# Optimization experiments

Hardware: AMD Instinct MI355X
Metric: run time of the kernel (lower is better)

## Reference

```python
import jax, jax.numpy as jnp
import numpy as np

D_DYN = 256    # dynamic_dim
D_STAT = 64    # static_dim
U_DIM = 48     # config.model.u_dim
N_OBS = 80     # num_prod*2 + num_inj = 32*2 + 16
T = 128        # rollout steps
B = 2048       # batch


def setup_inputs() -> dict:
    key = jax.random.key(0)
    k = jax.random.split(key, 8)
    z_dyn = jax.random.normal(k[0], (B, D_DYN), dtype=jnp.float32)
    z_static = jax.random.normal(k[1], (B, D_STAT), dtype=jnp.float32)
    dt = jnp.ones((1,), dtype=jnp.float32) * 0.05
    U = jax.random.normal(k[2], (T, B, U_DIM), dtype=jnp.float32)
    # learned params, initialized as in the torch module
    eig_raw = jnp.zeros((D_DYN,), dtype=jnp.float32)
    V = jnp.eye(D_DYN, dtype=jnp.float32) + jax.random.normal(k[3], (D_DYN, D_DYN), dtype=jnp.float32) * 0.01
    L = jax.random.normal(k[4], (D_DYN, U_DIM), dtype=jnp.float32) * (1.0 / np.sqrt(U_DIM))
    C = jax.random.normal(k[5], (N_OBS, D_DYN), dtype=jnp.float32) * (1.0 / np.sqrt(D_DYN))
    Dm = jax.random.normal(k[6], (N_OBS, U_DIM), dtype=jnp.float32) * (1.0 / np.sqrt(U_DIM))
    return {"z_dyn": z_dyn, "z_static": z_static, "dt": dt, "U": U,
            "eig_raw": eig_raw, "V": V, "L": L, "C": C, "Dm": Dm}


def reference(z_dyn, z_static, dt, U, eig_raw, V, L, C, Dm):
    # Stable Koopman operator: K = V diag(sigmoid(eig_raw)*0.99) V^{-1}
    eigvals = jax.nn.sigmoid(eig_raw) * 0.99
    K = (V * eigvals[None, :]) @ jnp.linalg.inv(V)  # [d, d]
    KT, LT, CT, DT = K.T, L.T, C.T, Dm.T
    dts = dt[0]

    def step(z, ut):
        ut_dt = ut * dts                 # [B, u_dim]
        z = z @ KT + ut_dt @ LT          # [B, d]
        y = z @ CT + ut_dt @ DT          # [B, n_obs]
        return z, (z, y)

    _, (Z, Y) = jax.lax.scan(step, z_dyn, U)
    return Z, Y  # [T, B, d], [T, B, n_obs]
```

## Files before the change

kernel.cpp:

```cpp
#include <hip/hip_runtime.h>

#define D_   256
#define UD_  48
#define NO_  80
#define T_   128
#define B_   2048

typedef __bf16 bf16x8 __attribute__((ext_vector_type(8)));
typedef float  f32x4  __attribute__((ext_vector_type(4)));
typedef unsigned short ushort_t;

static __device__ __forceinline__ ushort_t f2bf(float f){
  return __builtin_bit_cast(ushort_t, (__bf16)f);
}
static __device__ __forceinline__ float bf2f(ushort_t u){
  union { unsigned int i; float f; } c; c.i = ((unsigned int)u) << 16; return c.f;
}
static __device__ __forceinline__ f32x4 mfma16(bf16x8 a, bf16x8 b, f32x4 c){
  return __builtin_amdgcn_mfma_f32_16x16x32_bf16(a, b, c, 0, 0, 0);
}


__global__ void k_init(const float* __restrict__ V, const float* __restrict__ eig,
                       float* __restrict__ Xa, float* __restrict__ lam){
  const int i = blockIdx.x, j = threadIdx.x;
  Xa[i*D_ + j] = (i == j ? 2.0f : 0.0f) - V[i*D_ + j];
  if (j == 0) lam[i] = 0.99f / (1.0f + expf(-eig[i]));
}

__global__ void k_mm_mul(const float* __restrict__ A, const float* __restrict__ B,
                         float* __restrict__ Cm){
  const int i = blockIdx.x, j = threadIdx.x;
  const float* Ar = A + i*D_;
  float a0=0.f,a1=0.f,a2=0.f,a3=0.f;
  #pragma unroll 4
  for (int k = 0; k < D_; k += 4){
    a0 += Ar[k+0] * B[(k+0)*D_ + j];
    a1 += Ar[k+1] * B[(k+1)*D_ + j];
    a2 += Ar[k+2] * B[(k+2)*D_ + j];
    a3 += Ar[k+3] * B[(k+3)*D_ + j];
  }
  Cm[i*D_ + j] = (a0+a1)+(a2+a3);
}

__global__ void k_mm_upd(const float* __restrict__ X, const float* __restrict__ Tm,
                         float* __restrict__ Xn){
  const int i = blockIdx.x, j = threadIdx.x;
  const float* Xr = X + i*D_;
  float a0=0.f,a1=0.f,a2=0.f,a3=0.f;
  #pragma unroll 4
  for (int k = 0; k < D_; k += 4){
    a0 += Xr[k+0] * Tm[(k+0)*D_ + j];
    a1 += Xr[k+1] * Tm[(k+1)*D_ + j];
    a2 += Xr[k+2] * Tm[(k+2)*D_ + j];
    a3 += Xr[k+3] * Tm[(k+3)*D_ + j];
  }
  Xn[i*D_ + j] = 2.0f*Xr[j] - ((a0+a1)+(a2+a3));
}

__global__ void k_prep1(const float* __restrict__ Vinv, const float* __restrict__ V,
                        const float* __restrict__ Lm, const float* __restrict__ Cmat,
                        const float* __restrict__ dt,
                        float* __restrict__ VinvT, float* __restrict__ Lw,
                        float* __restrict__ Cw, float* __restrict__ dVd){
  const int bid = blockIdx.x, tid = threadIdx.x;
  if (bid < 256){
    VinvT[tid*D_ + bid] = Vinv[bid*D_ + tid];
    if (tid == bid){ float v = V[bid*D_ + bid]; dVd[bid] = v - bf2f(f2bf(v)); }
  } else if (bid < 512){
    const int i = bid - 256;
    if (tid < UD_){
      float acc = 0.f;
      #pragma unroll 4
      for (int j = 0; j < D_; ++j) acc += Vinv[i*D_ + j] * Lm[j*UD_ + tid];
      Lw[i*UD_ + tid] = acc * dt[0];
    }
  } else {
    const int n = bid - 512;
    float acc = 0.f;
    #pragma unroll 4
    for (int j = 0; j < D_; ++j) acc += Cmat[n*D_ + j] * V[j*D_ + tid];
    Cw[n*D_ + tid] = acc;
  }
}

__global__ void k_prep2(const float* __restrict__ z0, const float* __restrict__ VinvT,
                        const float* __restrict__ Lw,
                        ushort_t* __restrict__ Wchk, ushort_t* __restrict__ Lws){
  __shared__ float zr[8][256];
  const int bid = blockIdx.x, tid = threadIdx.x;
  if (bid < 256){
    const int b0 = bid * 8;
    #pragma unroll
    for (int r = 0; r < 8; ++r) zr[r][tid] = z0[(size_t)(b0+r)*D_ + tid];
    __syncthreads();
    float acc[8] = {0.f,0.f,0.f,0.f,0.f,0.f,0.f,0.f};
    #pragma unroll 4
    for (int j = 0; j < D_; ++j){
      const float vj = VinvT[j*D_ + tid];
      #pragma unroll
      for (int r = 0; r < 8; ++r) acc[r] += zr[r][j] * vj;
    }
    #pragma unroll
    for (int r = 0; r < 8; ++r)
      Wchk[(size_t)(b0+r)*D_ + tid] = f2bf(acc[r]);
    return;
  }
  const int f = bid - 256;
  if (tid >= 64) return;
  const int l = tid, lm = l & 15, lh = l >> 4;
  const int it = f >> 1, kc2 = f & 1;
  const int ig = it*16 + lm;
  #pragma unroll
  for (int j = 0; j < 8; ++j){
    const int k = 32*kc2 + 4*lh + (j & 3) + 16*(j >> 2);
    Lws[(f*64 + l)*8 + j] = f2bf(k < UD_ ? Lw[ig*UD_ + k] : 0.f);
  }
}

__global__ void k_packA(const float* __restrict__ V, const float* __restrict__ Cw,
                        const float* __restrict__ Dmat, const float* __restrict__ dt,
                        ushort_t* __restrict__ Af){
  const int mt = blockIdx.x / 10, kc = blockIdx.x % 10;
  const int l = threadIdx.x, lm = l & 15, lh = l >> 4;
  const float dts = dt[0];
  #pragma unroll
  for (int j = 0; j < 8; ++j){
    const int k = 32*kc + 4*lh + (j & 3) + 16*(j >> 2);
    float val = 0.f;
    if (mt < 16){
      if (kc < 8) val = V[(mt*16 + lm)*D_ + k];
    } else {
      const int n = (mt - 16)*16 + lm;
      if (kc < 8) val = Cw[n*D_ + k];
      else { const int ku = k - 256; if (ku < UD_) val = dts * Dmat[n*UD_ + ku]; }
    }
    Af[((size_t)(mt*10 + kc)*64 + l)*8 + j] = f2bf(val);
  }
}

#define SCAN_STEP(UA, UB, UC, TT) do {                                          \
  union { ushort_t us[8]; bf16x8 v; } c0, c1;                                   \
  c0.us[0]=f2bf((UA).x); c0.us[1]=f2bf((UA).y); c0.us[2]=f2bf((UA).z); c0.us[3]=f2bf((UA).w); \
  c0.us[4]=f2bf((UB).x); c0.us[5]=f2bf((UB).y); c0.us[6]=f2bf((UB).z); c0.us[7]=f2bf((UB).w); \
  c1.us[0]=f2bf((UC).x); c1.us[1]=f2bf((UC).y); c1.us[2]=f2bf((UC).z); c1.us[3]=f2bf((UC).w); \
  c1.us[4]=0; c1.us[5]=0; c1.us[6]=0; c1.us[7]=0;                               \
  _Pragma("unroll")                                                             \
  for (int q = 0; q < 2; ++q){                                                  \
    f32x4 acc = {0.f,0.f,0.f,0.f};                                              \
    acc = mfma16(lwf[q*2+0], c0.v, acc);                                        \
    acc = mfma16(lwf[q*2+1], c1.v, acc);                                        \
    _Pragma("unroll")                                                           \
    for (int r = 0; r < 4; ++r) w[q*4+r] = lamr[q*4+r]*w[q*4+r] + acc[r];       \
  }                                                                             \
  if ((((TT) & 7) == 7) && ((TT) < T_-1)){                                      \
    const int c2 = ((TT)+1) >> 3;                                               \
    _Pragma("unroll")                                                           \
    for (int q = 0; q < 2; ++q){                                                \
      const int i = (itb+q)*16 + 4*lh;                                          \
      ushort4 o; o.x=f2bf(w[q*4+0]); o.y=f2bf(w[q*4+1]); o.z=f2bf(w[q*4+2]); o.w=f2bf(w[q*4+3]); \
      *(ushort4*)(Wchk + ((size_t)c2*B_ + row)*D_ + i) = o;                     \
    }                                                                           \
  }                                                                             \
} while(0)

__global__ void __launch_bounds__(256) k_scan(const float* __restrict__ U,
    const ushort_t* __restrict__ Lws, const float* __restrict__ lam,
    ushort_t* __restrict__ Wchk){
  const int tid = threadIdx.x;
  const int wid = tid >> 6, l = tid & 63;
  const int lm = l & 15, lh = l >> 4;
  const int bq = blockIdx.x >> 1, ih = blockIdx.x & 1;
  const int b0 = bq * 16;
  const int row = b0 + lm;
  const int itb = ih*8 + wid*2;

  bf16x8 lwf[4];
  #pragma unroll
  for (int q = 0; q < 2; ++q)
    #pragma unroll
    for (int c = 0; c < 2; ++c)
      lwf[q*2 + c] = *(const bf16x8*)(Lws + ((size_t)(((itb+q)*2 + c)*64 + l))*8);

  float lamr[8], w[8];
  #pragma unroll
  for (int q = 0; q < 2; ++q){
    const int i = (itb+q)*16 + 4*lh;
    const float4 lv = *(const float4*)&lam[i];
    const ushort4 wu = *(const ushort4*)(Wchk + (size_t)row*D_ + i);
    lamr[q*4+0]=lv.x; lamr[q*4+1]=lv.y; lamr[q*4+2]=lv.z; lamr[q*4+3]=lv.w;
    w[q*4+0]=bf2f(wu.x); w[q*4+1]=bf2f(wu.y); w[q*4+2]=bf2f(wu.z); w[q*4+3]=bf2f(wu.w);
  }

  const size_t TS = (size_t)B_ * UD_;
  const float* Urow = U + (size_t)row * UD_;
  float4 Aa, Ab, Ac, Ba, Bb, Bc;
  Aa = *(const float4*)&Urow[4*lh]; Ab = *(const float4*)&Urow[16+4*lh]; Ac = *(const float4*)&Urow[32+4*lh];
  { const float* Up = Urow + TS;
    Ba = *(const float4*)&Up[4*lh]; Bb = *(const float4*)&Up[16+4*lh]; Bc = *(const float4*)&Up[32+4*lh]; }

  #pragma unroll 1
  for (int tt = 0; tt < 64; ++tt){
    const int t0 = 2*tt;
    SCAN_STEP(Aa, Ab, Ac, t0);
    if (t0 + 2 < T_){
      const float* Up = Urow + (size_t)(t0+2)*TS;
      Aa = *(const float4*)&Up[4*lh]; Ab = *(const float4*)&Up[16+4*lh]; Ac = *(const float4*)&Up[32+4*lh];
    }
    SCAN_STEP(Ba, Bb, Bc, t0+1);
    if (t0 + 3 < T_){
      const float* Up = Urow + (size_t)(t0+3)*TS;
      Ba = *(const float4*)&Up[4*lh]; Bb = *(const float4*)&Up[16+4*lh]; Bc = *(const float4*)&Up[32+4*lh];
    }
  }
}

__global__ void __launch_bounds__(256) k_fused(
    const float* __restrict__ U, const ushort_t* __restrict__ Af,
    const ushort_t* __restrict__ Lws, const float* __restrict__ lam,
    const float* __restrict__ dVd, const ushort_t* __restrict__ Wchk,
    float* __restrict__ outZ, float* __restrict__ outY){
  __shared__ __align__(16) ushort_t AfZhL[8*8*512];
  __shared__ __align__(16) ushort_t LwsL[32*512];
  __shared__ __align__(16) ushort_t AfYhL[30*512];
  __shared__ __align__(16) float    trbZ[4][16][68];
  __shared__ __align__(16) float    dVdL[128];
  __shared__ __align__(16) float    lamL[256];

  const int tid = threadIdx.x;
  const int bid = blockIdx.x;
  const int h  = bid >> 9;
  const int ch = bid & 15;
  const int bq = (bid >> 4) & 31;
  const int wid = tid >> 6, l = tid & 63;
  const int lm = l & 15, lh = l >> 4;
  const int col0 = bq*64 + wid*16;
  const int col = col0 + lm;

  {
    const uint4* gsrc = (const uint4*)Af;
    uint4* dz = (uint4*)AfZhL;
    #pragma unroll
    for (int r = 0; r < 16; ++r){
      const int i = r*256 + tid;
      const int f = i >> 6, l4 = i & 63;
      const int mi8 = f >> 3, kc = f & 7;
      dz[i] = gsrc[(size_t)((h*8 + mi8)*10 + kc)*64 + l4];
    }
    uint4* dy = (uint4*)AfYhL;
    const int nY = h ? 1280 : 1920;
    const int sb = 16 + (h ? 3 : 0);
    #pragma unroll
    for (int r = 0; r < 8; ++r){
      const int i = r*256 + tid;
      if (i < nY){
        const int f = i >> 6, l4 = i & 63;
        const int myl = f / 10, j = f % 10;
        dy[i] = gsrc[(size_t)((sb + myl)*10 + j)*64 + l4];
      }
    }
    const uint4* ls = (const uint4*)Lws;
    uint4* ld = (uint4*)LwsL;
    #pragma unroll
    for (int r = 0; r < 8; ++r) ld[r*256 + tid] = ls[r*256 + tid];
    if (tid < 32) ((float4*)dVdL)[tid] = ((const float4*)(dVd + h*128))[tid];
    else if (tid < 96) ((float4*)lamL)[tid-32] = ((const float4*)lam)[tid-32];
  }

  float w[64];
  #pragma unroll
  for (int kc = 0; kc < 8; ++kc)
    #pragma unroll
    for (int hh = 0; hh < 2; ++hh){
      const int i = 32*kc + 16*hh + 4*lh;
      const ushort4 wu = *(const ushort4*)(Wchk + ((size_t)ch*B_ + col)*D_ + i);
      const int e = 8*kc + 4*hh;
      w[e+0]=bf2f(wu.x); w[e+1]=bf2f(wu.y); w[e+2]=bf2f(wu.z); w[e+3]=bf2f(wu.w);
    }

  const size_t TS = (size_t)B_ * UD_;
  const float* Ucol = U + (size_t)col * UD_;
  float4 ua, ub, uc;
  {
    const float* Ut = Ucol + (size_t)(ch*8)*TS;
    ua = *(const float4*)&Ut[4*lh]; ub = *(const float4*)&Ut[16+4*lh]; uc = *(const float4*)&Ut[32+4*lh];
  }

  __syncthreads();

#define ZLOOP(HH)                                                               \
  { float* zbase = outZ + ((size_t)t*B_ + col0)*D_ + (HH)*128;                  \
    _Pragma("unroll")                                                           \
    for (int g = 0; g < 2; ++g){                                                \
      _Pragma("unroll")                                                         \
      for (int mi = 0; mi < 4; ++mi){                                           \
        const int mi8 = g*4 + mi;                                               \
        f32x4 acc = {0.f,0.f,0.f,0.f};                                          \
        _Pragma("unroll")                                                       \
        for (int kc = 0; kc < 8; ++kc){                                         \
          const bf16x8 af = *(const bf16x8*)&AfZhL[((mi8*8+kc)*64 + l)*8];      \
          acc = mfma16(af, wfr[kc], acc);                                       \
        }                                                                       \
        const float4 dv = *(const float4*)&dVdL[mi8*16 + 4*lh];                 \
        acc[0] += dv.x * (float)wfr[((HH)*8+mi8)>>1][0 + 4*(mi8&1)];            \
        acc[1] += dv.y * (float)wfr[((HH)*8+mi8)>>1][1 + 4*(mi8&1)];            \
        acc[2] += dv.z * (float)wfr[((HH)*8+mi8)>>1][2 + 4*(mi8&1)];            \
        acc[3] += dv.w * (float)wfr[((HH)*8+mi8)>>1][3 + 4*(mi8&1)];            \
        *(float4*)&trbZ[wid][lm][mi*16 + 4*lh] = make_float4(acc[0],acc[1],acc[2],acc[3]); \
      }                                                                         \
      __builtin_amdgcn_wave_barrier();                                          \
      _Pragma("unroll")                                                         \
      for (int j = 0; j < 4; ++j){                                              \
        const int r_ = j*4 + (l >> 4), c16 = l & 15;                            \
        const float4 v = *(const float4*)&trbZ[wid][r_][4*c16];                 \
        *(float4*)&zbase[(size_t)r_*D_ + g*64 + 4*c16] = v;                     \
      }                                                                         \
      __builtin_amdgcn_wave_barrier();                                          \
    } }

#define YLOOP(COFF, NMY)                                                        \
  { float* yrow = outY + ((size_t)t*B_ + col)*NO_ + (COFF);                     \
    _Pragma("unroll")                                                           \
    for (int my = 0; my < (NMY); ++my){                                         \
      f32x4 acc = {0.f,0.f,0.f,0.f};                                            \
      _Pragma("unroll")                                                         \
      for (int kc = 0; kc < 8; ++kc){                                           \
        const bf16x8 af = *(const bf16x8*)&AfYhL[((my*10+kc)*64 + l)*8];        \
        acc = mfma16(af, wfr[kc], acc);                                         \
      }                                                                         \
      { const bf16x8 af8 = *(const bf16x8*)&AfYhL[((my*10+8)*64 + l)*8];        \
        const bf16x8 af9 = *(const bf16x8*)&AfYhL[((my*10+9)*64 + l)*8];        \
        acc = mfma16(af8, uf0, acc); acc = mfma16(af9, uf1, acc); }             \
      *(float4*)&yrow[my*16 + 4*lh] = make_float4(acc[0],acc[1],acc[2],acc[3]); \
    } }

  #pragma unroll 1
  for (int s = 0; s < 8; ++s){
    const int t = ch*8 + s;
    bf16x8 uf0, uf1;
    {
      union { ushort_t us[8]; bf16x8 v; } cv;
      cv.us[0]=f2bf(ua.x); cv.us[1]=f2bf(ua.y); cv.us[2]=f2bf(ua.z); cv.us[3]=f2bf(ua.w);
      cv.us[4]=f2bf(ub.x); cv.us[5]=f2bf(ub.y); cv.us[6]=f2bf(ub.z); cv.us[7]=f2bf(ub.w);
      uf0 = cv.v;
      cv.us[0]=f2bf(uc.x); cv.us[1]=f2bf(uc.y); cv.us[2]=f2bf(uc.z); cv.us[3]=f2bf(uc.w);
      cv.us[4]=0; cv.us[5]=0; cv.us[6]=0; cv.us[7]=0;
      uf1 = cv.v;
    }
    if (s < 7){
      const float* Ut = Ucol + (size_t)(t+1)*TS;
      ua = *(const float4*)&Ut[4*lh]; ub = *(const float4*)&Ut[16+4*lh]; uc = *(const float4*)&Ut[32+4*lh];
    }
    #pragma unroll
    for (int it = 0; it < 16; ++it){
      const bf16x8 a0 = *(const bf16x8*)&LwsL[((it*2+0)*64 + l)*8];
      const bf16x8 a1 = *(const bf16x8*)&LwsL[((it*2+1)*64 + l)*8];
      const float4 lv = *(const float4*)&lamL[32*(it>>1) + 16*(it&1) + 4*lh];
      f32x4 acc = {0.f,0.f,0.f,0.f};
      acc = mfma16(a0, uf0, acc);
      acc = mfma16(a1, uf1, acc);
      const int e0 = 8*(it>>1) + 4*(it&1);
      w[e0+0] = lv.x*w[e0+0] + acc[0];
      w[e0+1] = lv.y*w[e0+1] + acc[1];
      w[e0+2] = lv.z*w[e0+2] + acc[2];
      w[e0+3] = lv.w*w[e0+3] + acc[3];
    }
    bf16x8 wfr[8];
    #pragma unroll
    for (int kc = 0; kc < 8; ++kc){
      union { ushort_t us[8]; bf16x8 v; } cv;
      #pragma unroll
      for (int j = 0; j < 8; ++j) cv.us[j] = f2bf(w[8*kc + j]);
      wfr[kc] = cv.v;
    }
    if (h == 0){
      ZLOOP(0);
      YLOOP(0, 3);
    } else {
      ZLOOP(1);
      YLOOP(48, 2);
    }
  }
#undef ZLOOP
#undef YLOOP
}

extern "C" void kernel_launch(void* const* d_in, const int* in_sizes, int n_in,
                              void* d_out, int out_size, void* d_ws, size_t ws_size,
                              hipStream_t stream){
  const float* z0  = (const float*)d_in[0];
  const float* dt  = (const float*)d_in[2];
  const float* U   = (const float*)d_in[3];
  const float* eig = (const float*)d_in[4];
  const float* V   = (const float*)d_in[5];
  const float* L   = (const float*)d_in[6];
  const float* C   = (const float*)d_in[7];
  const float* Dm  = (const float*)d_in[8];
  float* outZ = (float*)d_out;
  float* outY = outZ + (size_t)T_*B_*D_;

  char* ws = (char*)d_ws;
  float* Xa    = (float*)(ws + 0);
  float* Xb    = (float*)(ws + 262144);
  float* Tt    = (float*)(ws + 524288);
  float* Lw    = (float*)(ws + 786432);
  float* Cw    = (float*)(ws + 835584);
  float* lam   = (float*)(ws + 917504);
  float* dVd   = (float*)(ws + 918528);
  ushort_t* Af   = (ushort_t*)(ws + 919552);
  ushort_t* Lws  = (ushort_t*)(ws + 1134592);
  ushort_t* Wchk = (ushort_t*)(ws + 1167360);
  if (ws_size < 17944576u) return;

  k_init<<<256,256,0,stream>>>(V, eig, Xa, lam);
  k_mm_mul<<<256,256,0,stream>>>(V, Xa, Tt);
  k_mm_upd<<<256,256,0,stream>>>(Xa, Tt, Xb);
  k_mm_mul<<<256,256,0,stream>>>(V, Xb, Tt);
  k_mm_upd<<<256,256,0,stream>>>(Xb, Tt, Xa);
  k_mm_mul<<<256,256,0,stream>>>(V, Xa, Tt);
  k_mm_upd<<<256,256,0,stream>>>(Xa, Tt, Xb);
  k_prep1<<<592,256,0,stream>>>(Xb, V, L, C, dt, Xa, Lw, Cw, dVd);
  k_prep2<<<288,256,0,stream>>>(z0, Xa, Lw, Wchk, Lws);
  k_packA<<<210,64,0,stream>>>(V, Cw, Dm, dt, Af);
  k_scan<<<256,256,0,stream>>>(U, Lws, lam, Wchk);
  k_fused<<<1024,256,0,stream>>>(U, Af, Lws, lam, dVd, Wchk, outZ, outY);
}
```

Measured before the change: 267.8 us.

## Fuse prep kernels, reformulate Newton inverse, rebalance scan and fused work split

Collapses the Newton-Schulz inverse setup: the first iteration is expanded algebraically (X1 = 4I - 6V + 4V^2 - V^3), and the transpose plus the L projection are folded into the last update, which cuts the number of small prep launches. The packing kernels are merged into one. The scan gives each block the full 256-wide state (4 tiles per wave, 128 blocks) instead of splitting it across two blocks. The fused kernel now interleaves the two halves across adjacent block ids and rebalances the Y tiles to 4 and 1. The aim is less launch overhead and better load balance, at the cost of halving scan parallelism and doubling its per-thread register state.

```diff
diff --git a/kernel.cpp b/kernel.cpp
--- a/kernel.cpp
+++ b/kernel.cpp
@@ -21,15 +21,56 @@
 }
 
 
-__global__ void k_init(const float* __restrict__ V, const float* __restrict__ eig,
-                       float* __restrict__ Xa, float* __restrict__ lam){
+__global__ void __launch_bounds__(256) k_pre(
+    const float* __restrict__ V, const float* __restrict__ eig,
+    const float* __restrict__ Cmat,
+    float* __restrict__ W, float* __restrict__ Cw,
+    float* __restrict__ lam, float* __restrict__ dVd){
+  const int bid = blockIdx.x, tid = threadIdx.x;
+  if (bid < 256){
+    const float* Ar = V + bid*D_;
+    float a0=0.f,a1=0.f,a2=0.f,a3=0.f;
+    #pragma unroll 4
+    for (int k = 0; k < D_; k += 4){
+      a0 += Ar[k+0] * V[(k+0)*D_ + tid];
+      a1 += Ar[k+1] * V[(k+1)*D_ + tid];
+      a2 += Ar[k+2] * V[(k+2)*D_ + tid];
+      a3 += Ar[k+3] * V[(k+3)*D_ + tid];
+    }
+    W[bid*D_ + tid] = (a0+a1)+(a2+a3);
+  } else if (bid < 256 + NO_){
+    const int n = bid - 256;
+    float acc = 0.f;
+    #pragma unroll 4
+    for (int j = 0; j < D_; ++j) acc += Cmat[n*D_ + j] * V[j*D_ + tid];
+    Cw[n*D_ + tid] = acc;
+  } else {
+    lam[tid] = 0.99f / (1.0f + expf(-eig[tid]));
+    const float v = V[tid*D_ + tid];
+    dVd[tid] = v - bf2f(f2bf(v));
+  }
+}
+
+__global__ void __launch_bounds__(256) k_x1(
+    const float* __restrict__ V, const float* __restrict__ W,
+    float* __restrict__ X1){
   const int i = blockIdx.x, j = threadIdx.x;
-  Xa[i*D_ + j] = (i == j ? 2.0f : 0.0f) - V[i*D_ + j];
-  if (j == 0) lam[i] = 0.99f / (1.0f + expf(-eig[i]));
-}
-
-__global__ void k_mm_mul(const float* __restrict__ A, const float* __restrict__ B,
-                         float* __restrict__ Cm){
+  const float* Ar = V + i*D_;
+  float a0=0.f,a1=0.f,a2=0.f,a3=0.f;
+  #pragma unroll 4
+  for (int k = 0; k < D_; k += 4){
+    a0 += Ar[k+0] * W[(k+0)*D_ + j];
+    a1 += Ar[k+1] * W[(k+1)*D_ + j];
+    a2 += Ar[k+2] * W[(k+2)*D_ + j];
+    a3 += Ar[k+3] * W[(k+3)*D_ + j];
+  }
+  X1[i*D_ + j] = (i == j ? 4.0f : 0.0f) - 6.0f*V[i*D_ + j] + 4.0f*W[i*D_ + j]
+                 - ((a0+a1)+(a2+a3));
+}
+
+__global__ void __launch_bounds__(256) k_mm_mul(
+    const float* __restrict__ A, const float* __restrict__ B,
+    float* __restrict__ Cm){
   const int i = blockIdx.x, j = threadIdx.x;
   const float* Ar = A + i*D_;
   float a0=0.f,a1=0.f,a2=0.f,a3=0.f;
@@ -43,10 +84,13 @@
   Cm[i*D_ + j] = (a0+a1)+(a2+a3);
 }
 
-__global__ void k_mm_upd(const float* __restrict__ X, const float* __restrict__ Tm,
-                         float* __restrict__ Xn){
+__global__ void __launch_bounds__(256) k_x2(
+    const float* __restrict__ X1, const float* __restrict__ Tm,
+    const float* __restrict__ Lmat, const float* __restrict__ dt,
+    float* __restrict__ VinvT, float* __restrict__ Lw){
+  __shared__ float row[256];
   const int i = blockIdx.x, j = threadIdx.x;
-  const float* Xr = X + i*D_;
+  const float* Xr = X1 + i*D_;
   float a0=0.f,a1=0.f,a2=0.f,a3=0.f;
   #pragma unroll 4
   for (int k = 0; k < D_; k += 4){
@@ -55,38 +99,25 @@
     a2 += Xr[k+2] * Tm[(k+2)*D_ + j];
     a3 += Xr[k+3] * Tm[(k+3)*D_ + j];
   }
-  Xn[i*D_ + j] = 2.0f*Xr[j] - ((a0+a1)+(a2+a3));
-}
-
-__global__ void k_prep1(const float* __restrict__ Vinv, const float* __restrict__ V,
-                        const float* __restrict__ Lm, const float* __restrict__ Cmat,
-                        const float* __restrict__ dt,
-                        float* __restrict__ VinvT, float* __restrict__ Lw,
-                        float* __restrict__ Cw, float* __restrict__ dVd){
-  const int bid = blockIdx.x, tid = threadIdx.x;
-  if (bid < 256){
-    VinvT[tid*D_ + bid] = Vinv[bid*D_ + tid];
-    if (tid == bid){ float v = V[bid*D_ + bid]; dVd[bid] = v - bf2f(f2bf(v)); }
-  } else if (bid < 512){
-    const int i = bid - 256;
-    if (tid < UD_){
-      float acc = 0.f;
-      #pragma unroll 4
-      for (int j = 0; j < D_; ++j) acc += Vinv[i*D_ + j] * Lm[j*UD_ + tid];
-      Lw[i*UD_ + tid] = acc * dt[0];
-    }
-  } else {
-    const int n = bid - 512;
+  const float out = 2.0f*Xr[j] - ((a0+a1)+(a2+a3));
+  VinvT[j*D_ + i] = out;
+  row[j] = out;
+  __syncthreads();
+  if (j < UD_){
     float acc = 0.f;
     #pragma unroll 4
-    for (int j = 0; j < D_; ++j) acc += Cmat[n*D_ + j] * V[j*D_ + tid];
-    Cw[n*D_ + tid] = acc;
-  }
-}
-
-__global__ void k_prep2(const float* __restrict__ z0, const float* __restrict__ VinvT,
-                        const float* __restrict__ Lw,
-                        ushort_t* __restrict__ Wchk, ushort_t* __restrict__ Lws){
+    for (int k = 0; k < D_; ++k) acc += row[k] * Lmat[k*UD_ + j];
+    Lw[i*UD_ + j] = acc * dt[0];
+  }
+}
+
+__global__ void __launch_bounds__(256) k_prep2(
+    const float* __restrict__ z0, const float* __restrict__ VinvT,
+    const float* __restrict__ Lw, const float* __restrict__ V,
+    const float* __restrict__ Cw, const float* __restrict__ Dmat,
+    const float* __restrict__ dt,
+    ushort_t* __restrict__ Wchk, ushort_t* __restrict__ Lws,
+    ushort_t* __restrict__ Af){
   __shared__ float zr[8][256];
   const int bid = blockIdx.x, tid = threadIdx.x;
   if (bid < 256){
@@ -104,49 +135,49 @@
     #pragma unroll
     for (int r = 0; r < 8; ++r)
       Wchk[(size_t)(b0+r)*D_ + tid] = f2bf(acc[r]);
-    return;
-  }
-  const int f = bid - 256;
-  if (tid >= 64) return;
-  const int l = tid, lm = l & 15, lh = l >> 4;
-  const int it = f >> 1, kc2 = f & 1;
-  const int ig = it*16 + lm;
-  #pragma unroll
-  for (int j = 0; j < 8; ++j){
-    const int k = 32*kc2 + 4*lh + (j & 3) + 16*(j >> 2);
-    Lws[(f*64 + l)*8 + j] = f2bf(k < UD_ ? Lw[ig*UD_ + k] : 0.f);
-  }
-}
-
-__global__ void k_packA(const float* __restrict__ V, const float* __restrict__ Cw,
-                        const float* __restrict__ Dmat, const float* __restrict__ dt,
-                        ushort_t* __restrict__ Af){
-  const int mt = blockIdx.x / 10, kc = blockIdx.x % 10;
-  const int l = threadIdx.x, lm = l & 15, lh = l >> 4;
-  const float dts = dt[0];
-  #pragma unroll
-  for (int j = 0; j < 8; ++j){
-    const int k = 32*kc + 4*lh + (j & 3) + 16*(j >> 2);
-    float val = 0.f;
-    if (mt < 16){
-      if (kc < 8) val = V[(mt*16 + lm)*D_ + k];
-    } else {
-      const int n = (mt - 16)*16 + lm;
-      if (kc < 8) val = Cw[n*D_ + k];
-      else { const int ku = k - 256; if (ku < UD_) val = dts * Dmat[n*UD_ + ku]; }
-    }
-    Af[((size_t)(mt*10 + kc)*64 + l)*8 + j] = f2bf(val);
-  }
-}
-
-#define SCAN_STEP(UA, UB, UC, TT) do {                                          \
+  } else if (bid < 288){
+    const int f = bid - 256;
+    if (tid < 64){
+      const int l = tid, lm = l & 15, lh = l >> 4;
+      const int it = f >> 1, kc2 = f & 1;
+      const int ig = it*16 + lm;
+      #pragma unroll
+      for (int j = 0; j < 8; ++j){
+        const int k = 32*kc2 + 4*lh + (j & 3) + 16*(j >> 2);
+        Lws[(f*64 + l)*8 + j] = f2bf(k < UD_ ? Lw[ig*UD_ + k] : 0.f);
+      }
+    }
+  } else {
+    const int v = (bid - 288)*4 + (tid >> 6);
+    if (v < 210){
+      const int mt = v / 10, kc = v % 10;
+      const int l = tid & 63, lm = l & 15, lh = l >> 4;
+      const float dts = dt[0];
+      #pragma unroll
+      for (int j = 0; j < 8; ++j){
+        const int k = 32*kc + 4*lh + (j & 3) + 16*(j >> 2);
+        float val = 0.f;
+        if (mt < 16){
+          if (kc < 8) val = V[(mt*16 + lm)*D_ + k];
+        } else {
+          const int n = (mt - 16)*16 + lm;
+          if (kc < 8) val = Cw[n*D_ + k];
+          else { const int ku = k - 256; if (ku < UD_) val = dts * Dmat[n*UD_ + ku]; }
+        }
+        Af[((size_t)(mt*10 + kc)*64 + l)*8 + j] = f2bf(val);
+      }
+    }
+  }
+}
+
+#define SCAN_STEP4(UA, UB, UC, TT) do {                                         \
   union { ushort_t us[8]; bf16x8 v; } c0, c1;                                   \
   c0.us[0]=f2bf((UA).x); c0.us[1]=f2bf((UA).y); c0.us[2]=f2bf((UA).z); c0.us[3]=f2bf((UA).w); \
   c0.us[4]=f2bf((UB).x); c0.us[5]=f2bf((UB).y); c0.us[6]=f2bf((UB).z); c0.us[7]=f2bf((UB).w); \
   c1.us[0]=f2bf((UC).x); c1.us[1]=f2bf((UC).y); c1.us[2]=f2bf((UC).z); c1.us[3]=f2bf((UC).w); \
   c1.us[4]=0; c1.us[5]=0; c1.us[6]=0; c1.us[7]=0;                               \
   _Pragma("unroll")                                                             \
-  for (int q = 0; q < 2; ++q){                                                  \
+  for (int q = 0; q < 4; ++q){                                                  \
     f32x4 acc = {0.f,0.f,0.f,0.f};                                              \
     acc = mfma16(lwf[q*2+0], c0.v, acc);                                        \
     acc = mfma16(lwf[q*2+1], c1.v, acc);                                        \
@@ -156,7 +187,7 @@
   if ((((TT) & 7) == 7) && ((TT) < T_-1)){                                      \
     const int c2 = ((TT)+1) >> 3;                                               \
     _Pragma("unroll")                                                           \
-    for (int q = 0; q < 2; ++q){                                                \
+    for (int q = 0; q < 4; ++q){                                                \
       const int i = (itb+q)*16 + 4*lh;                                          \
       ushort4 o; o.x=f2bf(w[q*4+0]); o.y=f2bf(w[q*4+1]); o.z=f2bf(w[q*4+2]); o.w=f2bf(w[q*4+3]); \
       *(ushort4*)(Wchk + ((size_t)c2*B_ + row)*D_ + i) = o;                     \
@@ -170,21 +201,20 @@
   const int tid = threadIdx.x;
   const int wid = tid >> 6, l = tid & 63;
   const int lm = l & 15, lh = l >> 4;
-  const int bq = blockIdx.x >> 1, ih = blockIdx.x & 1;
-  const int b0 = bq * 16;
+  const int b0 = blockIdx.x * 16;
   const int row = b0 + lm;
-  const int itb = ih*8 + wid*2;
-
-  bf16x8 lwf[4];
+  const int itb = wid*4;
+
+  bf16x8 lwf[8];
   #pragma unroll
-  for (int q = 0; q < 2; ++q)
+  for (int q = 0; q < 4; ++q)
     #pragma unroll
     for (int c = 0; c < 2; ++c)
       lwf[q*2 + c] = *(const bf16x8*)(Lws + ((size_t)(((itb+q)*2 + c)*64 + l))*8);
 
-  float lamr[8], w[8];
+  float lamr[16], w[16];
   #pragma unroll
-  for (int q = 0; q < 2; ++q){
+  for (int q = 0; q < 4; ++q){
     const int i = (itb+q)*16 + 4*lh;
     const float4 lv = *(const float4*)&lam[i];
     const ushort4 wu = *(const ushort4*)(Wchk + (size_t)row*D_ + i);
@@ -202,12 +232,12 @@
   #pragma unroll 1
   for (int tt = 0; tt < 64; ++tt){
     const int t0 = 2*tt;
-    SCAN_STEP(Aa, Ab, Ac, t0);
+    SCAN_STEP4(Aa, Ab, Ac, t0);
     if (t0 + 2 < T_){
       const float* Up = Urow + (size_t)(t0+2)*TS;
       Aa = *(const float4*)&Up[4*lh]; Ab = *(const float4*)&Up[16+4*lh]; Ac = *(const float4*)&Up[32+4*lh];
     }
-    SCAN_STEP(Ba, Bb, Bc, t0+1);
+    SCAN_STEP4(Ba, Bb, Bc, t0+1);
     if (t0 + 3 < T_){
       const float* Up = Urow + (size_t)(t0+3)*TS;
       Ba = *(const float4*)&Up[4*lh]; Bb = *(const float4*)&Up[16+4*lh]; Bc = *(const float4*)&Up[32+4*lh];
@@ -222,16 +252,16 @@
     float* __restrict__ outZ, float* __restrict__ outY){
   __shared__ __align__(16) ushort_t AfZhL[8*8*512];
   __shared__ __align__(16) ushort_t LwsL[32*512];
-  __shared__ __align__(16) ushort_t AfYhL[30*512];
+  __shared__ __align__(16) ushort_t AfYhL[40*512];
   __shared__ __align__(16) float    trbZ[4][16][68];
   __shared__ __align__(16) float    dVdL[128];
   __shared__ __align__(16) float    lamL[256];
 
   const int tid = threadIdx.x;
   const int bid = blockIdx.x;
-  const int h  = bid >> 9;
-  const int ch = bid & 15;
-  const int bq = (bid >> 4) & 31;
+  const int h  = bid & 1;
+  const int ch = (bid >> 1) & 15;
+  const int bq = bid >> 5;
   const int wid = tid >> 6, l = tid & 63;
   const int lm = l & 15, lh = l >> 4;
   const int col0 = bq*64 + wid*16;
@@ -248,10 +278,10 @@
       dz[i] = gsrc[(size_t)((h*8 + mi8)*10 + kc)*64 + l4];
     }
     uint4* dy = (uint4*)AfYhL;
-    const int nY = h ? 1280 : 1920;
-    const int sb = 16 + (h ? 3 : 0);
-    #pragma unroll
-    for (int r = 0; r < 8; ++r){
+    const int nY = h ? 640 : 2560;
+    const int sb = 16 + (h ? 4 : 0);
+    #pragma unroll
+    for (int r = 0; r < 10; ++r){
       const int i = r*256 + tid;
       if (i < nY){
         const int f = i >> 6, l4 = i & 63;
@@ -375,10 +405,10 @@
     }
     if (h == 0){
       ZLOOP(0);
-      YLOOP(0, 3);
+      YLOOP(0, 4);
     } else {
       ZLOOP(1);
-      YLOOP(48, 2);
+      YLOOP(64, 1);
     }
   }
 #undef ZLOOP
@@ -412,16 +442,11 @@
   ushort_t* Wchk = (ushort_t*)(ws + 1167360);
   if (ws_size < 17944576u) return;
 
-  k_init<<<256,256,0,stream>>>(V, eig, Xa, lam);
-  k_mm_mul<<<256,256,0,stream>>>(V, Xa, Tt);
-  k_mm_upd<<<256,256,0,stream>>>(Xa, Tt, Xb);
+  k_pre   <<<337,256,0,stream>>>(V, eig, C, Xa, Cw, lam, dVd);
+  k_x1    <<<256,256,0,stream>>>(V, Xa, Xb);
   k_mm_mul<<<256,256,0,stream>>>(V, Xb, Tt);
-  k_mm_upd<<<256,256,0,stream>>>(Xb, Tt, Xa);
-  k_mm_mul<<<256,256,0,stream>>>(V, Xa, Tt);
-  k_mm_upd<<<256,256,0,stream>>>(Xa, Tt, Xb);
-  k_prep1<<<592,256,0,stream>>>(Xb, V, L, C, dt, Xa, Lw, Cw, dVd);
-  k_prep2<<<288,256,0,stream>>>(z0, Xa, Lw, Wchk, Lws);
-  k_packA<<<210,64,0,stream>>>(V, Cw, Dm, dt, Af);
-  k_scan<<<256,256,0,stream>>>(U, Lws, lam, Wchk);
-  k_fused<<<1024,256,0,stream>>>(U, Af, Lws, lam, dVd, Wchk, outZ, outY);
-}
+  k_x2    <<<256,256,0,stream>>>(Xb, Tt, L, dt, Xa, Lw);
+  k_prep2 <<<342,256,0,stream>>>(z0, Xa, Lw, V, Cw, Dm, dt, Wchk, Lws, Af);
+  k_scan  <<<128,256,0,stream>>>(U, Lws, lam, Wchk);
+  k_fused <<<1024,256,0,stream>>>(U, Af, Lws, lam, dVd, Wchk, outZ, outY);
+}
```

After: 279.7 us. 1.04x slower.
